# Performance work log

Hardware: AMD Instinct MI355X
Metric: run time of the kernel (lower is better)

The kernel has to match this reference:

```python
import jax, jax.numpy as jnp
import numpy as np

V, L_MAX, D_MODEL, N_LAYER, N_STATE, EXPAND = 49408, 512, 768, 4, 16, 2
D_INNER = EXPAND * D_MODEL            # 1536
DT_RANK = -(-D_MODEL // 16)           # 48 ('auto' = ceil(d_model/16))
D_CONV = 4
B, T = 4, 256
EPS = 1e-5


def setup_inputs() -> dict:
    key = jax.random.key(0)
    ks = jax.random.split(key, 10)
    s = 0.02
    inp = {
        "input_ids": jax.random.randint(ks[0], (B, T), 0, V),
        "emb": jax.random.normal(ks[1], (V, D_MODEL), jnp.float32) * s,
        "pos_emb": jax.random.normal(ks[2], (1, L_MAX, D_MODEL), jnp.float32) * s,
        "in_proj_w": jax.random.normal(ks[3], (N_LAYER, 2 * D_INNER, D_MODEL), jnp.float32) * s,
        "conv_w": jax.random.normal(ks[4], (N_LAYER, D_INNER, D_CONV), jnp.float32) * s,
        "conv_b": jnp.zeros((N_LAYER, D_INNER), jnp.float32),
        "x_proj_w": jax.random.normal(ks[5], (N_LAYER, DT_RANK + 2 * N_STATE, D_INNER), jnp.float32) * s,
        "dt_proj_w": jax.random.normal(ks[6], (N_LAYER, D_INNER, DT_RANK), jnp.float32) * s,
        "dt_proj_b": jnp.full((N_LAYER, D_INNER), -4.6, jnp.float32),  # softplus(-4.6)~0.01, inside [dt_min,dt_max]
        # S4D-real init: A_log[l,d,n] = log(n+1)
        "A_log": jnp.tile(jnp.log(jnp.arange(1, N_STATE + 1, dtype=jnp.float32)), (N_LAYER, D_INNER, 1)),
        "D_skip": jnp.ones((N_LAYER, D_INNER), jnp.float32),
        "out_proj_w": jax.random.normal(ks[7], (N_LAYER, D_MODEL, D_INNER), jnp.float32) * s,
        "norm_w": jnp.ones((D_MODEL,), jnp.float32),
    }
    return inp


def _causal_dwconv(x, w, b):
    # x: (B, C, T), w: (C, K) depthwise, b: (C,) ; causal pad K-1 on the left
    out = jax.lax.conv_general_dilated(
        x, w[:, None, :], window_strides=(1,), padding=[(D_CONV - 1, 0)],
        feature_group_count=x.shape[1], dimension_numbers=("NCH", "OIH", "NCH"))
    return out + b[None, :, None]


def _selective_scan(deltaA, dBx, Cm):
    # deltaA, dBx: (B, T, D, N); Cm: (B, T, N) -> y: (B, T, D)
    def step(h, t_in):
        dA, dbx, c = t_in
        h = dA * h + dbx                          # (B, D, N)
        y = jnp.einsum("bdn,bn->bd", h, c)
        return h, y
    h0 = jnp.zeros(deltaA.shape[:1] + deltaA.shape[2:], deltaA.dtype)
    _, ys = jax.lax.scan(step, h0, (deltaA.swapaxes(0, 1), dBx.swapaxes(0, 1), Cm.swapaxes(0, 1)))
    return ys.swapaxes(0, 1)


def _mamba_block(x, ipw, cw, cb, xpw, dpw, dpb, A_log, Dp, opw):
    # x: (B, T, d_model)
    xz = jnp.einsum("btd,ed->bte", x, ipw)        # (B, T, 2*D_INNER)
    xi, z = jnp.split(xz, 2, axis=-1)
    xi = jax.nn.silu(_causal_dwconv(xi.swapaxes(1, 2), cw, cb)).swapaxes(1, 2)  # (B, T, D_INNER)
    x_dbl = jnp.einsum("btd,ed->bte", xi, xpw)    # (B, T, DT_RANK + 2N)
    dt, Bm, Cm = jnp.split(x_dbl, [DT_RANK, DT_RANK + N_STATE], axis=-1)
    dt = jax.nn.softplus(jnp.einsum("btr,dr->btd", dt, dpw) + dpb)              # (B, T, D_INNER)
    A = -jnp.exp(A_log)                            # (D_INNER, N)
    deltaA = jnp.exp(dt[..., None] * A)            # (B, T, D_INNER, N)
    dBx = dt[..., None] * Bm[:, :, None, :] * xi[..., None]                     # (B, T, D_INNER, N)
    y = _selective_scan(deltaA, dBx, Cm) + Dp * xi
    y = y * jax.nn.silu(z)
    return jnp.einsum("btd,ed->bte", y, opw)       # (B, T, d_model)


def reference(input_ids, emb, pos_emb, in_proj_w, conv_w, conv_b, x_proj_w,
              dt_proj_w, dt_proj_b, A_log, D_skip, out_proj_w, norm_w):
    Tlen = input_ids.shape[1]
    x = emb[input_ids] + pos_emb[:, :Tlen, :]
    for l in range(N_LAYER):
        x = x + _mamba_block(x, in_proj_w[l], conv_w[l], conv_b[l], x_proj_w[l],
                             dt_proj_w[l], dt_proj_b[l], A_log[l], D_skip[l], out_proj_w[l])
    # RMSNormGated with no gate -> plain RMSNorm
    x = x * jax.lax.rsqrt(jnp.mean(x * x, axis=-1, keepdims=True) + EPS) * norm_w
    return x
```

## Files before the change

kernel.cpp:

```cpp
#include <hip/hip_runtime.h>
#include <math.h>

#define TLEN 256
#define BATCH 4
#define DMODEL 768
#define DINNER 1536
#define NSTATE 16
#define DTRANK 48
#define NLAYER 4
#define NTOK 1024

#define S_IP 2359296
#define S_OP 1179648
#define S_XP2 196608
#define S_DT 98304
#define WL (S_IP + S_OP + S_XP2 + S_DT)
#define NB_W (WL / 1024)
#define NB_WALL (NB_W * NLAYER)
#define NB_E (NTOK * DMODEL / 256)

typedef __bf16 bf16x8 __attribute__((ext_vector_type(8)));
typedef float f32x4 __attribute__((ext_vector_type(4)));

__device__ inline unsigned short f2b(float f) {
    union { float f; unsigned u; } v;
    v.f = f;
    unsigned r = (v.u + 0x7fffu + ((v.u >> 16) & 1u)) >> 16;
    return (unsigned short)r;
}
__device__ inline float b2f(unsigned short u) {
    union { unsigned u; float f; } v;
    v.u = ((unsigned)u) << 16;
    return v.f;
}

__device__ inline void gload16(const void* g, void* l) {
    __builtin_amdgcn_global_load_lds(
        (const __attribute__((address_space(1))) void*)g,
        (__attribute__((address_space(3))) void*)l, 16, 0, 0);
}

__device__ inline float red16(float p) {
    p += __int_as_float(__builtin_amdgcn_update_dpp(0, __float_as_int(p), 0xB1, 0xf, 0xf, true));
    p += __int_as_float(__builtin_amdgcn_update_dpp(0, __float_as_int(p), 0x4E, 0xf, 0xf, true));
    p += __int_as_float(__builtin_amdgcn_update_dpp(0, __float_as_int(p), 0x124, 0xf, 0xf, true));
    p += __int_as_float(__builtin_amdgcn_update_dpp(0, __float_as_int(p), 0x128, 0xf, 0xf, true));
    return p;
}

__global__ __launch_bounds__(256) void prep_k(const float* __restrict__ ipw,
                                              const float* __restrict__ opw,
                                              const float* __restrict__ xpw,
                                              const float* __restrict__ dpw,
                                              const int* __restrict__ ids,
                                              const float* __restrict__ emb,
                                              const float* __restrict__ pos,
                                              unsigned short* __restrict__ w_all,
                                              float* __restrict__ x,
                                              unsigned short* __restrict__ xb) {
    int bid = blockIdx.x;
    int tid = threadIdx.x;
    if (bid >= NB_WALL) {
        int idx = (bid - NB_WALL) * 256 + tid;
        int d = idx % DMODEL;
        int bt = idx / DMODEL;
        int t = bt % TLEN;
        float v = emb[(size_t)ids[bt] * DMODEL + d] + pos[t * DMODEL + d];
        x[idx] = v;
        xb[idx] = f2b(v);
        return;
    }
    int l = bid / NB_W;
    int i4 = ((bid % NB_W) * 256 + tid) * 4;
    unsigned short* wl = w_all + (size_t)l * WL;
    if (i4 < S_IP) {
        float4 v = *(const float4*)(ipw + (size_t)l * S_IP + i4);
        ushort4 o; o.x = f2b(v.x); o.y = f2b(v.y); o.z = f2b(v.z); o.w = f2b(v.w);
        *(ushort4*)(wl + i4) = o;
    } else if (i4 < S_IP + S_OP) {
        int i = i4 - S_IP;
        float4 v = *(const float4*)(opw + (size_t)l * S_OP + i);
        ushort4 o; o.x = f2b(v.x); o.y = f2b(v.y); o.z = f2b(v.z); o.w = f2b(v.w);
        *(ushort4*)(wl + S_IP + i) = o;
    } else if (i4 < S_IP + S_OP + S_XP2) {
        int i = i4 - S_IP - S_OP;
        int r = i / 1536, k = i % 1536;
        ushort4 o = {0, 0, 0, 0};
        if (r < 80) {
            float4 v = *(const float4*)(xpw + (size_t)l * (80 * 1536) + (size_t)r * 1536 + k);
            o.x = f2b(v.x); o.y = f2b(v.y); o.z = f2b(v.z); o.w = f2b(v.w);
        }
        *(ushort4*)(wl + S_IP + S_OP + i) = o;
    } else {
        int i = i4 - S_IP - S_OP - S_XP2;
        int r = i >> 6, k = i & 63;
        ushort4 o = {0, 0, 0, 0};
        if (k < DTRANK) {
            float4 v = *(const float4*)(dpw + (size_t)l * (DINNER * DTRANK) + (size_t)r * DTRANK + k);
            o.x = f2b(v.x); o.y = f2b(v.y); o.z = f2b(v.z); o.w = f2b(v.w);
        }
        *(ushort4*)(wl + S_IP + S_OP + S_XP2 + i) = o;
    }
}

__global__ __launch_bounds__(256) void ipgemm_k(const unsigned short* __restrict__ A,
                                                const unsigned short* __restrict__ B,
                                                unsigned short* __restrict__ o1) {
    __shared__ __align__(16) unsigned short Ab[2][128 * 64];
    __shared__ __align__(16) unsigned short Bb[2][128 * 64];

    int tid = threadIdx.x;
    int lane = tid & 63;
    int wave = tid >> 6;
    int wm = (wave >> 1) * 64;
    int wn = (wave & 1) * 64;
    int bm = blockIdx.x * 128;
    int bn = blockIdx.y * 128;
    int fr = lane & 15;
    int fq = lane >> 4;
    int fk = fq * 8;
    int srow = lane >> 3;
    int scol = (lane & 7) * 8;

    f32x4 acc[4][4] = {};

    auto stage = [&](int s, int k0) {
#pragma unroll
        for (int c = 0; c < 4; ++c) {
            int r = wave * 32 + c * 8;
            gload16(A + (size_t)(bm + r + srow) * DMODEL + k0 + scol, &Ab[s][r * 64]);
            gload16(B + (size_t)(bn + r + srow) * DMODEL + k0 + scol, &Bb[s][r * 64]);
        }
    };

    const int nk = DMODEL / 64;
    stage(0, 0);
    asm volatile("s_waitcnt vmcnt(0)" ::: "memory");
    __builtin_amdgcn_s_barrier();

    for (int t = 0; t < nk; ++t) {
        int cur = t & 1;
        if (t + 1 < nk) stage(cur ^ 1, (t + 1) * 64);
#pragma unroll
        for (int ks = 0; ks < 2; ++ks) {
            int kk = ks * 32 + fk;
            bf16x8 af[4], bfr[4];
#pragma unroll
            for (int i = 0; i < 4; ++i)
                af[i] = *(const bf16x8*)&Ab[cur][(wm + i * 16 + fr) * 64 + kk];
#pragma unroll
            for (int j = 0; j < 4; ++j)
                bfr[j] = *(const bf16x8*)&Bb[cur][(wn + j * 16 + fr) * 64 + kk];
#pragma unroll
            for (int i = 0; i < 4; ++i)
#pragma unroll
                for (int j = 0; j < 4; ++j)
                    acc[i][j] = __builtin_amdgcn_mfma_f32_16x16x32_bf16(
                        af[i], bfr[j], acc[i][j], 0, 0, 0);
        }
        asm volatile("s_waitcnt vmcnt(0)" ::: "memory");
        __builtin_amdgcn_s_barrier();
    }

#pragma unroll
    for (int i = 0; i < 4; ++i) {
#pragma unroll
        for (int j = 0; j < 4; ++j) {
            int lc = wn + j * 16 + fr;
#pragma unroll
            for (int q = 0; q < 4; ++q) {
                int lr = wm + i * 16 + fq * 4 + q;
                o1[(size_t)(bm + lr) * NTOK + bn + lc] = f2b(acc[i][j][q]);
            }
        }
    }
}

template <int MODE>
__global__ __launch_bounds__(256) void mgemm_k(const unsigned short* __restrict__ A, int lda,
                                               const unsigned short* __restrict__ B, int ldb,
                                               int K,
                                               const float* __restrict__ bias,
                                               float* __restrict__ o0,
                                               unsigned short* __restrict__ o1) {
    __shared__ __align__(16) unsigned short Ab[2][64 * 64];
    __shared__ __align__(16) unsigned short Bb[2][64 * 64];
    __shared__ float Tt[(MODE == 1) ? 64 * 64 : 1];

    int tid = threadIdx.x;
    int lane = tid & 63;
    int wave = tid >> 6;
    int wm = (wave >> 1) * 32;
    int wn = (wave & 1) * 32;
    int bm = blockIdx.x * 64;
    int bn = blockIdx.y * 64;
    int fr = lane & 15;
    int fq = lane >> 4;
    int fk = fq * 8;
    int srow = lane >> 3;
    int scol = (lane & 7) * 8;

    f32x4 acc[2][2] = {};

    auto stage = [&](int s, int k0) {
#pragma unroll
        for (int c = 0; c < 2; ++c) {
            int r = wave * 16 + c * 8;
            gload16(A + (size_t)(bm + r + srow) * lda + k0 + scol, &Ab[s][r * 64]);
            gload16(B + (size_t)(bn + r + srow) * ldb + k0 + scol, &Bb[s][r * 64]);
        }
    };

    int nk = K >> 6;
    stage(0, 0);
    asm volatile("s_waitcnt vmcnt(0)" ::: "memory");
    __builtin_amdgcn_s_barrier();

    for (int t = 0; t < nk; ++t) {
        int cur = t & 1;
        if (t + 1 < nk) stage(cur ^ 1, (t + 1) * 64);
#pragma unroll
        for (int ks = 0; ks < 2; ++ks) {
            int kk = ks * 32 + fk;
            bf16x8 af[2], bfr[2];
#pragma unroll
            for (int i = 0; i < 2; ++i)
                af[i] = *(const bf16x8*)&Ab[cur][(wm + i * 16 + fr) * 64 + kk];
#pragma unroll
            for (int j = 0; j < 2; ++j)
                bfr[j] = *(const bf16x8*)&Bb[cur][(wn + j * 16 + fr) * 64 + kk];
#pragma unroll
            for (int i = 0; i < 2; ++i)
#pragma unroll
                for (int j = 0; j < 2; ++j)
                    acc[i][j] = __builtin_amdgcn_mfma_f32_16x16x32_bf16(
                        af[i], bfr[j], acc[i][j], 0, 0, 0);
        }
        asm volatile("s_waitcnt vmcnt(0)" ::: "memory");
        __builtin_amdgcn_s_barrier();
    }

#pragma unroll
    for (int i = 0; i < 2; ++i) {
#pragma unroll
        for (int j = 0; j < 2; ++j) {
            int lc = wn + j * 16 + fr;
#pragma unroll
            for (int q = 0; q < 4; ++q) {
                int lr = wm + i * 16 + fq * 4 + q;
                float v = acc[i][j][q];
                if (MODE == 1) {
                    int f = bm + lr;
                    if (f >= DTRANK && f < 80) o0[(size_t)f * NTOK + bn + lc] = v;
                    Tt[lc * 64 + lr] = v;
                } else if (MODE == 2) {
                    float s = v + bias[bm + lr];
                    s = (s > 0.f) ? s + log1pf(__expf(-s)) : log1pf(__expf(s));
                    o1[(size_t)(bm + lr) * NTOK + bn + lc] = f2b(s);
                } else if (MODE == 3) {
                    size_t idx = (size_t)(bm + lr) * DMODEL + bn + lc;
                    float nv = o0[idx] + v;
                    o0[idx] = nv;
                    o1[idx] = f2b(nv);
                }
            }
        }
    }
    if (MODE == 1) {
        __syncthreads();
        if (bm == 0) {
            int tok = tid >> 2;
            int fb = (tid & 3) * 16;
#pragma unroll
            for (int vv = 0; vv < 4; ++vv) {
                int f0 = fb + vv * 4;
                ushort4 o;
                o.x = f2b(Tt[tok * 64 + f0 + 0]);
                o.y = f2b(Tt[tok * 64 + f0 + 1]);
                o.z = f2b(Tt[tok * 64 + f0 + 2]);
                o.w = f2b(Tt[tok * 64 + f0 + 3]);
                *(ushort4*)(o1 + (size_t)(bn + tok) * 64 + f0) = o;
            }
        }
    }
}

__global__ __launch_bounds__(256) void conv_k(const unsigned short* __restrict__ xzT,
                                              const float* __restrict__ cw,
                                              const float* __restrict__ cb,
                                              unsigned short* __restrict__ xib) {
    __shared__ unsigned short tile[4][256];
    int tid = threadIdx.x;
    int ch = tid >> 6;
    int d = blockIdx.x * 4 + ch;
    int b = blockIdx.y;
    int t0 = (tid & 63) * 4;
    const unsigned short* src = xzT + (size_t)d * NTOK + b * TLEN + t0;
    ushort4 cur = *(const ushort4*)src;
    ushort4 prev = {0, 0, 0, 0};
    if (t0 > 0) prev = *(const ushort4*)(src - 4);
    float w0 = cw[d * 4 + 0], w1 = cw[d * 4 + 1], w2 = cw[d * 4 + 2], w3 = cw[d * 4 + 3];
    float bb = cb[d];
    float xw[8] = {b2f(prev.x), b2f(prev.y), b2f(prev.z), b2f(prev.w),
                   b2f(cur.x), b2f(cur.y), b2f(cur.z), b2f(cur.w)};
#pragma unroll
    for (int u = 0; u < 4; ++u) {
        float s = bb + w0 * xw[u + 1] + w1 * xw[u + 2] + w2 * xw[u + 3] + w3 * xw[u + 4];
        float v = s / (1.f + __expf(-s));
        tile[ch][t0 + u] = f2b(v);
    }
    __syncthreads();
    int t = tid;
    ushort4 o;
    o.x = tile[0][t]; o.y = tile[1][t]; o.z = tile[2][t]; o.w = tile[3][t];
    *(ushort4*)(xib + (size_t)(b * TLEN + t) * DINNER + blockIdx.x * 4) = o;
}

__global__ __launch_bounds__(512) void scan_k(const unsigned short* __restrict__ dtT,
                                              const unsigned short* __restrict__ xzT,
                                              const float* __restrict__ xdblT,
                                              const float* __restrict__ cw,
                                              const float* __restrict__ cb,
                                              const float* __restrict__ Alog,
                                              const float* __restrict__ Dsk,
                                              unsigned short* __restrict__ ybb) {
    __shared__ float yl[4][260];
    __shared__ float cum[4][260];
    __shared__ float hL[8][4][16];
    __shared__ float Pb[8][4][16];
    __shared__ float Hin[8][4][16];

    int tid = threadIdx.x;
    int c = tid >> 6;
    int lane = tid & 63;
    int ch = lane >> 4;
    int n = lane & 15;
    int d = blockIdx.x * 4 + ch;
    int b = blockIdx.y;
    int tl0 = c * 32;

    float a = -__expf(Alog[(size_t)d * NSTATE + n]);
    float Dv = Dsk[d];
    float w0 = cw[d * 4 + 0], w1 = cw[d * 4 + 1], w2 = cw[d * 4 + 2], w3 = cw[d * 4 + 3];
    float cbv = cb[d];
    const unsigned short* dtp = dtT + (size_t)d * NTOK + b * TLEN + tl0;
    const unsigned short* xzp = xzT + (size_t)d * NTOK + b * TLEN + tl0;
    const float* Bp = xdblT + (size_t)(DTRANK + n) * NTOK + b * TLEN + tl0;
    const float* Cp = xdblT + (size_t)(DTRANK + NSTATE + n) * NTOK + b * TLEN + tl0;

    float hm3 = 0.f, hm2 = 0.f, hm1 = 0.f;
    if (tl0 > 0) {
        ushort4 pv = *(const ushort4*)(xzp - 4);
        hm3 = b2f(pv.y); hm2 = b2f(pv.z); hm1 = b2f(pv.w);
    }

    float h = 0.f, cd = 0.f;
    for (int t8 = 0; t8 < 32; t8 += 8) {
        ushort4 dv0 = *(const ushort4*)(dtp + t8), dv1 = *(const ushort4*)(dtp + t8 + 4);
        ushort4 xv0 = *(const ushort4*)(xzp + t8), xv1 = *(const ushort4*)(xzp + t8 + 4);
        float4 B0 = *(const float4*)(Bp + t8), B1 = *(const float4*)(Bp + t8 + 4);
        float4 C0 = *(const float4*)(Cp + t8), C1 = *(const float4*)(Cp + t8 + 4);
        float dts[8] = {b2f(dv0.x), b2f(dv0.y), b2f(dv0.z), b2f(dv0.w),
                        b2f(dv1.x), b2f(dv1.y), b2f(dv1.z), b2f(dv1.w)};
        float xw[11] = {hm3, hm2, hm1,
                        b2f(xv0.x), b2f(xv0.y), b2f(xv0.z), b2f(xv0.w),
                        b2f(xv1.x), b2f(xv1.y), b2f(xv1.z), b2f(xv1.w)};
        float Bs[8] = {B0.x, B0.y, B0.z, B0.w, B1.x, B1.y, B1.z, B1.w};
        float Cs[8] = {C0.x, C0.y, C0.z, C0.w, C1.x, C1.y, C1.z, C1.w};
#pragma unroll
        for (int u = 0; u < 8; ++u) {
            float sv = cbv + w0 * xw[u] + w1 * xw[u + 1] + w2 * xw[u + 2] + w3 * xw[u + 3];
            float xi = sv / (1.f + __expf(-sv));
            float dtv = dts[u];
            cd += dtv;
            float dA = __expf(dtv * a);
            h = dA * h + (dtv * xi) * Bs[u];
            float p = red16(h * Cs[u]);
            if (n == 0) {
                yl[ch][tl0 + t8 + u] = p + Dv * xi;
                cum[ch][tl0 + t8 + u] = cd;
            }
        }
        hm3 = xw[8]; hm2 = xw[9]; hm1 = xw[10];
    }
    hL[c][ch][n] = h;
    Pb[c][ch][n] = __expf(a * cd);
    __syncthreads();
    if (c == 0) {
        float H = 0.f;
        Hin[0][ch][n] = 0.f;
#pragma unroll
        for (int cc = 1; cc < 8; ++cc) {
            H = Pb[cc - 1][ch][n] * H + hL[cc - 1][ch][n];
            Hin[cc][ch][n] = H;
        }
    }
    __syncthreads();
    float Hv = Hin[c][ch][n];
    const unsigned short* zp = xzT + (size_t)(DINNER + d) * NTOK + b * TLEN + tl0;
    for (int t8 = 0; t8 < 32; t8 += 8) {
        float4 C0 = *(const float4*)(Cp + t8), C1 = *(const float4*)(Cp + t8 + 4);
        ushort4 zv0 = *(const ushort4*)(zp + t8), zv1 = *(const ushort4*)(zp + t8 + 4);
        float Cs[8] = {C0.x, C0.y, C0.z, C0.w, C1.x, C1.y, C1.z, C1.w};
        float zs[8] = {b2f(zv0.x), b2f(zv0.y), b2f(zv0.z), b2f(zv0.w),
                       b2f(zv1.x), b2f(zv1.y), b2f(zv1.z), b2f(zv1.w)};
#pragma unroll
        for (int u = 0; u < 8; ++u) {
            float cdt = cum[ch][tl0 + t8 + u];
            float corr = red16(Cs[u] * __expf(a * cdt) * Hv);
            if (n == 0) {
                float y = yl[ch][tl0 + t8 + u] + corr;
                float zz = zs[u];
                y *= zz / (1.f + __expf(-zz));
                yl[ch][tl0 + t8 + u] = y;
            }
        }
    }
    __syncthreads();
    if (tid < 256) {
        int t = tid;
        ushort4 o;
        o.x = f2b(yl[0][t]);
        o.y = f2b(yl[1][t]);
        o.z = f2b(yl[2][t]);
        o.w = f2b(yl[3][t]);
        *(ushort4*)(ybb + (size_t)(b * TLEN + t) * DINNER + blockIdx.x * 4) = o;
    }
}

__global__ __launch_bounds__(256) void rmsnorm_k(const float* __restrict__ x,
                                                 const float* __restrict__ nw,
                                                 float* __restrict__ out) {
    int row = blockIdx.x;
    const float* xr = x + (size_t)row * DMODEL;
    int tid = threadIdx.x;
    float s = 0.f;
    for (int d = tid; d < DMODEL; d += 256) {
        float v = xr[d];
        s += v * v;
    }
#pragma unroll
    for (int off = 32; off >= 1; off >>= 1) s += __shfl_down(s, off);
    __shared__ float red[4];
    __shared__ float scale;
    int wid = tid >> 6, lane = tid & 63;
    if (lane == 0) red[wid] = s;
    __syncthreads();
    if (tid == 0) {
        float tot = red[0] + red[1] + red[2] + red[3];
        scale = rsqrtf(tot / (float)DMODEL + 1e-5f);
    }
    __syncthreads();
    float sc = scale;
    for (int d = tid; d < DMODEL; d += 256)
        out[(size_t)row * DMODEL + d] = xr[d] * sc * nw[d];
}

extern "C" void kernel_launch(void* const* d_in, const int* in_sizes, int n_in,
                              void* d_out, int out_size, void* d_ws, size_t ws_size,
                              hipStream_t stream) {
    const int* ids = (const int*)d_in[0];
    const float* emb = (const float*)d_in[1];
    const float* pos = (const float*)d_in[2];
    const float* ipw = (const float*)d_in[3];
    const float* cw = (const float*)d_in[4];
    const float* cb = (const float*)d_in[5];
    const float* xpw = (const float*)d_in[6];
    const float* dpw = (const float*)d_in[7];
    const float* dpb = (const float*)d_in[8];
    const float* Alog = (const float*)d_in[9];
    const float* Dsk = (const float*)d_in[10];
    const float* opw = (const float*)d_in[11];
    const float* nw = (const float*)d_in[12];

    float* x = (float*)d_ws;
    float* xdblT = x + 786432;
    unsigned short* xb = (unsigned short*)(xdblT + 81920);
    unsigned short* xzT = xb + 786432;
    unsigned short* xib = xzT + 3145728;
    unsigned short* dtT = xib + 1572864;
    unsigned short* ybb = dtT + 1572864;
    unsigned short* xdblb = ybb + 1572864;
    unsigned short* w_all = xdblb + 65536;

    prep_k<<<NB_WALL + NB_E, 256, 0, stream>>>(ipw, opw, xpw, dpw, ids, emb, pos,
                                               w_all, x, xb);

    for (int l = 0; l < NLAYER; ++l) {
        const unsigned short* w_ip = w_all + (size_t)l * WL;
        const unsigned short* w_op = w_ip + S_IP;
        const unsigned short* w_xp = w_op + S_OP;
        const unsigned short* w_dt = w_xp + S_XP2;
        const float* cw_l = cw + (size_t)l * DINNER * 4;
        const float* cb_l = cb + (size_t)l * DINNER;
        const float* dpb_l = dpb + (size_t)l * DINNER;
        const float* Alog_l = Alog + (size_t)l * DINNER * NSTATE;
        const float* Dsk_l = Dsk + (size_t)l * DINNER;

        ipgemm_k<<<dim3(3072 / 128, NTOK / 128), 256, 0, stream>>>(w_ip, xb, xzT);
        conv_k<<<dim3(DINNER / 4, BATCH), 256, 0, stream>>>(xzT, cw_l, cb_l, xib);
        mgemm_k<1><<<dim3(2, NTOK / 64), 256, 0, stream>>>(
            w_xp, DINNER, xib, DINNER, DINNER, nullptr, xdblT, xdblb);
        mgemm_k<2><<<dim3(DINNER / 64, NTOK / 64), 256, 0, stream>>>(
            w_dt, 64, xdblb, 64, 64, dpb_l, nullptr, dtT);
        scan_k<<<dim3(DINNER / 4, BATCH), 512, 0, stream>>>(
            dtT, xzT, xdblT, cw_l, cb_l, Alog_l, Dsk_l, ybb);
        mgemm_k<3><<<dim3(NTOK / 64, DMODEL / 64), 256, 0, stream>>>(
            ybb, DINNER, w_op, DINNER, DINNER, nullptr, x, xb);
    }

    rmsnorm_k<<<NTOK, 256, 0, stream>>>(x, nw, (float*)d_out);
}
```

Measured before the change: 521.6 us.

## Fuse dt projection and softplus into the scan kernel prologue

Measured after the change: 511.9 us. No clear change (-1.9%).

```diff
diff --git a/kernel.cpp b/kernel.cpp
--- a/kernel.cpp
+++ b/kernel.cpp
@@ -13,8 +13,7 @@
 #define S_IP 2359296
 #define S_OP 1179648
 #define S_XP2 196608
-#define S_DT 98304
-#define WL (S_IP + S_OP + S_XP2 + S_DT)
+#define WL (S_IP + S_OP + S_XP2)
 #define NB_W (WL / 1024)
 #define NB_WALL (NB_W * NLAYER)
 #define NB_E (NTOK * DMODEL / 256)
@@ -51,7 +50,6 @@
 __global__ __launch_bounds__(256) void prep_k(const float* __restrict__ ipw,
                                               const float* __restrict__ opw,
                                               const float* __restrict__ xpw,
-                                              const float* __restrict__ dpw,
                                               const int* __restrict__ ids,
                                               const float* __restrict__ emb,
                                               const float* __restrict__ pos,
@@ -82,7 +80,7 @@
         float4 v = *(const float4*)(opw + (size_t)l * S_OP + i);
         ushort4 o; o.x = f2b(v.x); o.y = f2b(v.y); o.z = f2b(v.z); o.w = f2b(v.w);
         *(ushort4*)(wl + S_IP + i) = o;
-    } else if (i4 < S_IP + S_OP + S_XP2) {
+    } else {
         int i = i4 - S_IP - S_OP;
         int r = i / 1536, k = i % 1536;
         ushort4 o = {0, 0, 0, 0};
@@ -91,15 +89,6 @@
             o.x = f2b(v.x); o.y = f2b(v.y); o.z = f2b(v.z); o.w = f2b(v.w);
         }
         *(ushort4*)(wl + S_IP + S_OP + i) = o;
-    } else {
-        int i = i4 - S_IP - S_OP - S_XP2;
-        int r = i >> 6, k = i & 63;
-        ushort4 o = {0, 0, 0, 0};
-        if (k < DTRANK) {
-            float4 v = *(const float4*)(dpw + (size_t)l * (DINNER * DTRANK) + (size_t)r * DTRANK + k);
-            o.x = f2b(v.x); o.y = f2b(v.y); o.z = f2b(v.z); o.w = f2b(v.w);
-        }
-        *(ushort4*)(wl + S_IP + S_OP + S_XP2 + i) = o;
     }
 }
 
@@ -180,12 +169,10 @@
 __global__ __launch_bounds__(256) void mgemm_k(const unsigned short* __restrict__ A, int lda,
                                                const unsigned short* __restrict__ B, int ldb,
                                                int K,
-                                               const float* __restrict__ bias,
                                                float* __restrict__ o0,
                                                unsigned short* __restrict__ o1) {
     __shared__ __align__(16) unsigned short Ab[2][64 * 64];
     __shared__ __align__(16) unsigned short Bb[2][64 * 64];
-    __shared__ float Tt[(MODE == 1) ? 64 * 64 : 1];
 
     int tid = threadIdx.x;
     int lane = tid & 63;
@@ -251,35 +238,13 @@
                 float v = acc[i][j][q];
                 if (MODE == 1) {
                     int f = bm + lr;
-                    if (f >= DTRANK && f < 80) o0[(size_t)f * NTOK + bn + lc] = v;
-                    Tt[lc * 64 + lr] = v;
-                } else if (MODE == 2) {
-                    float s = v + bias[bm + lr];
-                    s = (s > 0.f) ? s + log1pf(__expf(-s)) : log1pf(__expf(s));
-                    o1[(size_t)(bm + lr) * NTOK + bn + lc] = f2b(s);
-                } else if (MODE == 3) {
+                    if (f < 80) o0[(size_t)f * NTOK + bn + lc] = v;
+                } else {
                     size_t idx = (size_t)(bm + lr) * DMODEL + bn + lc;
                     float nv = o0[idx] + v;
                     o0[idx] = nv;
                     o1[idx] = f2b(nv);
                 }
-            }
-        }
-    }
-    if (MODE == 1) {
-        __syncthreads();
-        if (bm == 0) {
-            int tok = tid >> 2;
-            int fb = (tid & 3) * 16;
-#pragma unroll
-            for (int vv = 0; vv < 4; ++vv) {
-                int f0 = fb + vv * 4;
-                ushort4 o;
-                o.x = f2b(Tt[tok * 64 + f0 + 0]);
-                o.y = f2b(Tt[tok * 64 + f0 + 1]);
-                o.z = f2b(Tt[tok * 64 + f0 + 2]);
-                o.w = f2b(Tt[tok * 64 + f0 + 3]);
-                *(ushort4*)(o1 + (size_t)(bn + tok) * 64 + f0) = o;
             }
         }
     }
@@ -316,14 +281,17 @@
     *(ushort4*)(xib + (size_t)(b * TLEN + t) * DINNER + blockIdx.x * 4) = o;
 }
 
-__global__ __launch_bounds__(512) void scan_k(const unsigned short* __restrict__ dtT,
-                                              const unsigned short* __restrict__ xzT,
+__global__ __launch_bounds__(512) void scan_k(const unsigned short* __restrict__ xzT,
                                               const float* __restrict__ xdblT,
+                                              const float* __restrict__ dpw,
+                                              const float* __restrict__ dpb,
                                               const float* __restrict__ cw,
                                               const float* __restrict__ cb,
                                               const float* __restrict__ Alog,
                                               const float* __restrict__ Dsk,
                                               unsigned short* __restrict__ ybb) {
+    __shared__ float dt_s[4][256];
+    __shared__ float wdt_s[192];
     __shared__ float yl[4][260];
     __shared__ float cum[4][260];
     __shared__ float hL[8][4][16];
@@ -335,15 +303,38 @@
     int lane = tid & 63;
     int ch = lane >> 4;
     int n = lane & 15;
-    int d = blockIdx.x * 4 + ch;
+    int d0 = blockIdx.x * 4;
+    int d = d0 + ch;
     int b = blockIdx.y;
     int tl0 = c * 32;
+
+    if (tid < 192) wdt_s[tid] = dpw[(size_t)d0 * DTRANK + tid];
+    __syncthreads();
+    {
+        int dd = tid >> 7;
+        int tt = tid & 127;
+        const float* wrow = &wdt_s[dd * DTRANK];
+        const float* base = xdblT + (size_t)b * TLEN + tt;
+        float a0 = 0.f, a1 = 0.f;
+#pragma unroll 8
+        for (int k = 0; k < DTRANK; ++k) {
+            float w = wrow[k];
+            a0 += w * base[(size_t)k * NTOK];
+            a1 += w * base[(size_t)k * NTOK + 128];
+        }
+        float bias = dpb[d0 + dd];
+        float v0 = a0 + bias, v1 = a1 + bias;
+        v0 = (v0 > 0.f) ? v0 + log1pf(__expf(-v0)) : log1pf(__expf(v0));
+        v1 = (v1 > 0.f) ? v1 + log1pf(__expf(-v1)) : log1pf(__expf(v1));
+        dt_s[dd][tt] = v0;
+        dt_s[dd][tt + 128] = v1;
+    }
+    __syncthreads();
 
     float a = -__expf(Alog[(size_t)d * NSTATE + n]);
     float Dv = Dsk[d];
     float w0 = cw[d * 4 + 0], w1 = cw[d * 4 + 1], w2 = cw[d * 4 + 2], w3 = cw[d * 4 + 3];
     float cbv = cb[d];
-    const unsigned short* dtp = dtT + (size_t)d * NTOK + b * TLEN + tl0;
     const unsigned short* xzp = xzT + (size_t)d * NTOK + b * TLEN + tl0;
     const float* Bp = xdblT + (size_t)(DTRANK + n) * NTOK + b * TLEN + tl0;
     const float* Cp = xdblT + (size_t)(DTRANK + NSTATE + n) * NTOK + b * TLEN + tl0;
@@ -356,12 +347,9 @@
 
     float h = 0.f, cd = 0.f;
     for (int t8 = 0; t8 < 32; t8 += 8) {
-        ushort4 dv0 = *(const ushort4*)(dtp + t8), dv1 = *(const ushort4*)(dtp + t8 + 4);
         ushort4 xv0 = *(const ushort4*)(xzp + t8), xv1 = *(const ushort4*)(xzp + t8 + 4);
         float4 B0 = *(const float4*)(Bp + t8), B1 = *(const float4*)(Bp + t8 + 4);
         float4 C0 = *(const float4*)(Cp + t8), C1 = *(const float4*)(Cp + t8 + 4);
-        float dts[8] = {b2f(dv0.x), b2f(dv0.y), b2f(dv0.z), b2f(dv0.w),
-                        b2f(dv1.x), b2f(dv1.y), b2f(dv1.z), b2f(dv1.w)};
         float xw[11] = {hm3, hm2, hm1,
                         b2f(xv0.x), b2f(xv0.y), b2f(xv0.z), b2f(xv0.w),
                         b2f(xv1.x), b2f(xv1.y), b2f(xv1.z), b2f(xv1.w)};
@@ -371,7 +359,7 @@
         for (int u = 0; u < 8; ++u) {
             float sv = cbv + w0 * xw[u] + w1 * xw[u + 1] + w2 * xw[u + 2] + w3 * xw[u + 3];
             float xi = sv / (1.f + __expf(-sv));
-            float dtv = dts[u];
+            float dtv = dt_s[ch][tl0 + t8 + u];
             cd += dtv;
             float dA = __expf(dtv * a);
             h = dA * h + (dtv * xi) * Bs[u];
@@ -478,21 +466,19 @@
     unsigned short* xb = (unsigned short*)(xdblT + 81920);
     unsigned short* xzT = xb + 786432;
     unsigned short* xib = xzT + 3145728;
-    unsigned short* dtT = xib + 1572864;
-    unsigned short* ybb = dtT + 1572864;
-    unsigned short* xdblb = ybb + 1572864;
-    unsigned short* w_all = xdblb + 65536;
-
-    prep_k<<<NB_WALL + NB_E, 256, 0, stream>>>(ipw, opw, xpw, dpw, ids, emb, pos,
+    unsigned short* ybb = xib + 1572864;
+    unsigned short* w_all = ybb + 1572864;
+
+    prep_k<<<NB_WALL + NB_E, 256, 0, stream>>>(ipw, opw, xpw, ids, emb, pos,
                                                w_all, x, xb);
 
     for (int l = 0; l < NLAYER; ++l) {
         const unsigned short* w_ip = w_all + (size_t)l * WL;
         const unsigned short* w_op = w_ip + S_IP;
         const unsigned short* w_xp = w_op + S_OP;
-        const unsigned short* w_dt = w_xp + S_XP2;
         const float* cw_l = cw + (size_t)l * DINNER * 4;
         const float* cb_l = cb + (size_t)l * DINNER;
+        const float* dpw_l = dpw + (size_t)l * DINNER * DTRANK;
         const float* dpb_l = dpb + (size_t)l * DINNER;
         const float* Alog_l = Alog + (size_t)l * DINNER * NSTATE;
         const float* Dsk_l = Dsk + (size_t)l * DINNER;
@@ -500,13 +486,11 @@
         ipgemm_k<<<dim3(3072 / 128, NTOK / 128), 256, 0, stream>>>(w_ip, xb, xzT);
         conv_k<<<dim3(DINNER / 4, BATCH), 256, 0, stream>>>(xzT, cw_l, cb_l, xib);
         mgemm_k<1><<<dim3(2, NTOK / 64), 256, 0, stream>>>(
-            w_xp, DINNER, xib, DINNER, DINNER, nullptr, xdblT, xdblb);
-        mgemm_k<2><<<dim3(DINNER / 64, NTOK / 64), 256, 0, stream>>>(
-            w_dt, 64, xdblb, 64, 64, dpb_l, nullptr, dtT);
+            w_xp, DINNER, xib, DINNER, DINNER, xdblT, nullptr);
         scan_k<<<dim3(DINNER / 4, BATCH), 512, 0, stream>>>(
-            dtT, xzT, xdblT, cw_l, cb_l, Alog_l, Dsk_l, ybb);
+            xzT, xdblT, dpw_l, dpb_l, cw_l, cb_l, Alog_l, Dsk_l, ybb);
         mgemm_k<3><<<dim3(NTOK / 64, DMODEL / 64), 256, 0, stream>>>(
-            ybb, DINNER, w_op, DINNER, DINNER, nullptr, x, xb);
+            ybb, DINNER, w_op, DINNER, DINNER, x, xb);
     }
 
     rmsnorm_k<<<NTOK, 256, 0, stream>>>(x, nw, (float*)d_out);
```
